# Performance work log

Hardware: AMD Instinct MI355X
Metric: run time of the kernel (lower is better)

Reference implementation:

```python
import jax, jax.numpy as jnp
import numpy as np

B, N, H, F_IN, F_OUT = 2048, 64, 4, 256, 256
NEG_SLOPE = 0.2


def setup_inputs() -> dict:
    key = jax.random.key(0)
    k1, k2, k3, k4 = jax.random.split(key, 4)
    return {
        "input": jax.random.normal(k1, (B, N, F_IN), dtype=jnp.float32),
        "adj": jax.random.uniform(k2, (B, N, N), dtype=jnp.float32),
        "W": jax.random.normal(k3, (F_IN, H * F_OUT), dtype=jnp.float32) * 0.05,
        "a_i": jax.random.normal(k4, (H, F_OUT), dtype=jnp.float32) * 0.05,
        "a_j": jax.random.normal(jax.random.fold_in(key, 5), (H, F_OUT), dtype=jnp.float32) * 0.05,
        "bias_param": jnp.zeros((H * F_OUT,), dtype=jnp.float32),
    }


def reference(input, adj, W, a_i, a_j, bias_param):
    # h: [B, N, H, F_OUT]
    h = (input @ W).reshape(B, N, H, F_OUT)
    # per-head attention coefficients (vectorized over heads)
    coeff_i = jnp.einsum("bnhf,hf->bnh", h, a_i)  # [B, N, H]
    coeff_j = jnp.einsum("bnhf,hf->bnh", h, a_j)  # [B, N, H]
    # e: [B, N(i), N(j), H]
    e = jax.nn.leaky_relu(coeff_i[:, :, None, :] + coeff_j[:, None, :, :],
                          negative_slope=NEG_SLOPE)
    adj4 = adj[..., None]  # [B, N, N, 1]
    # self_loop_type == 2: adj unchanged. Mask logits, softmax over j, re-mask.
    attention = jax.nn.softmax(e * adj4, axis=2) * adj4
    # dropout p = 0.0 / eval mode -> identity
    # weighted aggregate per head, then concat heads (average=False)
    out = jnp.einsum("bijh,bjhf->bihf", attention, h).reshape(B, N, H * F_OUT)
    return out + bias_param
```

## Files before the change

### kernel.cpp

```cpp
#include <hip/hip_runtime.h>

#define B_  2048
#define N_  64
#define H_  4
#define FI  256
#define FO  256
#define HF  1024

typedef _Float16 f16;
typedef _Float16 f16x8 __attribute__((ext_vector_type(8)));
typedef _Float16 f16x4 __attribute__((ext_vector_type(4)));
typedef float f32x4 __attribute__((ext_vector_type(4)));

#define MFMA16(a,b,c) __builtin_amdgcn_mfma_f32_16x16x32_f16(a, b, c, 0, 0, 0)

__global__ __launch_bounds__(256) void prep_w_kernel(const float* __restrict__ W,
                                                     f16* __restrict__ wfrag) {
    int tid  = blockIdx.x * 256 + threadIdx.x;
    int lane = tid & 63;
    int ctg  = (tid >> 6) & 63;
    int kt   = tid >> 12;
    int krow = kt * 32 + (lane >> 4) * 8;
    int col  = ctg * 16 + (lane & 15);
    f16x8 v;
#pragma unroll
    for (int j = 0; j < 8; ++j)
        v[j] = (f16)W[(size_t)(krow + j) * HF + col];
    *((f16x8*)wfrag + tid) = v;
}

#define SMEM_BYTES 51200
#define SADJ_OFF   32768
#define SCI_OFF    40960
#define SCJ_OFF    45056
#define SCIS_OFF   49152
#define SCJS_OFF   50176

__global__ __launch_bounds__(1024, 1) void gat_kernel(
    const float* __restrict__ input, const float* __restrict__ adj,
    const f16* __restrict__ wfrag, const float* __restrict__ a_i,
    const float* __restrict__ a_j, const float* __restrict__ bias,
    float* __restrict__ out)
{
    __shared__ unsigned char smem[SMEM_BYTES] __attribute__((aligned(16)));
    float* sCi  = (float*)(smem + SCI_OFF);
    float* sCj  = (float*)(smem + SCJ_OFF);
    float* sCiS = (float*)(smem + SCIS_OFF);
    float* sCjS = (float*)(smem + SCJS_OFF);

    const int b    = blockIdx.x;
    const int tid  = threadIdx.x;
    const int wv   = tid >> 6;
    const int w    = wv >> 2;
    const int ch2  = wv & 3;
    const int lane = tid & 63;
    const int g    = lane >> 4;
    const int c15  = lane & 15;

    {
        const float* inb = input + (size_t)b * (N_ * FI);
#pragma unroll
        for (int c = 0; c < 2; ++c) {
            int idx = tid + 1024 * c;
            int row = idx >> 5;
            int k0  = (idx & 31) << 3;
            const float4* p = (const float4*)(inb + row * FI + k0);
            float4 v0 = p[0], v1 = p[1];
            f16x8 h8;
            h8[0] = (f16)v0.x; h8[1] = (f16)v0.y; h8[2] = (f16)v0.z; h8[3] = (f16)v0.w;
            h8[4] = (f16)v1.x; h8[5] = (f16)v1.y; h8[6] = (f16)v1.z; h8[7] = (f16)v1.w;
            unsigned addr = (unsigned)(row * 512 + k0 * 2) ^ ((unsigned)(row & 7) << 4);
            *(f16x8*)(smem + addr) = h8;
        }
        if (tid < 512) {
            int i  = tid >> 3;
            int jb = tid & 7;
            const float* ap = adj + (size_t)b * (N_ * N_) + i * N_ + jb * 8;
            float4 q0 = ((const float4*)ap)[0];
            float4 q1 = ((const float4*)ap)[1];
            f16x4 lo, hi;
            lo[0] = (f16)q0.x; lo[1] = (f16)q0.y; lo[2] = (f16)q0.z; lo[3] = (f16)q0.w;
            hi[0] = (f16)q1.x; hi[1] = (f16)q1.y; hi[2] = (f16)q1.z; hi[3] = (f16)q1.w;
            unsigned k0p = (unsigned)(32 * (jb >> 2) + 16 * (jb & 1) + 4 * ((jb >> 1) & 1));
            unsigned sw  = (unsigned)(i & 7) << 4;
            *(f16x4*)(smem + SADJ_OFF + (((unsigned)(i * 128) + k0p * 2) ^ sw)) = lo;
            *(f16x4*)(smem + SADJ_OFF + (((unsigned)(i * 128) + (k0p + 8) * 2) ^ sw)) = hi;
        }
    }
    __syncthreads();

    float ciP[16], cjP[16];
#pragma unroll
    for (int q = 0; q < 16; ++q) { ciP[q] = 0.f; cjP[q] = 0.f; }
    f16x8 hB[2][4];

#pragma unroll
    for (int cc = 0; cc < 2; ++cc) {
        f32x4 acc[4][2];
#pragma unroll
        for (int rt = 0; rt < 4; ++rt)
#pragma unroll
            for (int ctl = 0; ctl < 2; ++ctl) {
                f32x4 z = {0.f, 0.f, 0.f, 0.f};
                acc[rt][ctl] = z;
            }
#pragma unroll
        for (int kt = 0; kt < 8; ++kt) {
            f16x8 aF[4];
#pragma unroll
            for (int rt = 0; rt < 4; ++rt) {
                int row = rt * 16 + c15;
                unsigned addr = ((unsigned)(row * 512 + (kt * 32 + g * 8) * 2))
                                ^ ((unsigned)(row & 7) << 4);
                aF[rt] = *(const f16x8*)(smem + addr);
            }
            f16x8 bF[2];
#pragma unroll
            for (int ctl = 0; ctl < 2; ++ctl) {
                int ctg = w * 16 + ch2 * 4 + cc * 2 + ctl;
                bF[ctl] = *((const f16x8*)wfrag + ((kt * 64 + ctg) * 64 + lane));
            }
#pragma unroll
            for (int rt = 0; rt < 4; ++rt)
#pragma unroll
                for (int ctl = 0; ctl < 2; ++ctl)
                    acc[rt][ctl] = MFMA16(aF[rt], bF[ctl], acc[rt][ctl]);
        }
#pragma unroll
        for (int ctl = 0; ctl < 2; ++ctl) {
            int ct = cc * 2 + ctl;
            int colg = w * FO + ch2 * 64 + ct * 16 + c15;
            float aIc = a_i[colg];
            float aJc = a_j[colg];
#pragma unroll
            for (int rt = 0; rt < 4; ++rt) {
#pragma unroll
                for (int r = 0; r < 4; ++r) {
                    float v = acc[rt][ctl][r];
                    ciP[rt * 4 + r] += v * aIc;
                    cjP[rt * 4 + r] += v * aJc;
                    hB[rt >> 1][ct][4 * (rt & 1) + r] = (f16)v;
                }
            }
        }
    }

#pragma unroll
    for (int s = 1; s < 16; s <<= 1) {
#pragma unroll
        for (int q = 0; q < 16; ++q) {
            ciP[q] += __shfl_xor(ciP[q], s);
            cjP[q] += __shfl_xor(cjP[q], s);
        }
    }
    if (c15 == 0) {
#pragma unroll
        for (int q = 0; q < 16; ++q) {
            int node = (q >> 2) * 16 + g * 4 + (q & 3);
            sCi[wv * 64 + node] = ciP[q];
            sCj[wv * 64 + node] = cjP[q];
        }
    }
    __syncthreads();

    if (tid < 512) {
        int wq    = tid >> 7;
        int which = (tid >> 6) & 1;
        int node  = tid & 63;
        const float* src = (which == 0 ? sCi : sCj) + (wq * 4) * 64 + node;
        float s = src[0] + src[64] + src[128] + src[192];
        (which == 0 ? sCiS : sCjS)[wq * 64 + node] = s;
    }
    __syncthreads();

#pragma unroll 1
    for (int it = 0; it < 4; ++it) {
        int i = it * 16 + c15;
        float ci = sCiS[w * 64 + i];
        unsigned sw = (unsigned)(i & 7) << 4;
        f16x8 adjv0 = *(const f16x8*)(smem + SADJ_OFF + (((unsigned)(i * 128) + (g * 8) * 2) ^ sw));
        f16x8 adjv1 = *(const f16x8*)(smem + SADJ_OFF + (((unsigned)(i * 128) + (32 + g * 8) * 2) ^ sw));
        float cj[16];
#pragma unroll
        for (int t = 0; t < 4; ++t) {
            float4 c4 = *(const float4*)(sCjS + w * 64 + t * 16 + 4 * g);
            cj[t * 4 + 0] = c4.x; cj[t * 4 + 1] = c4.y;
            cj[t * 4 + 2] = c4.z; cj[t * 4 + 3] = c4.w;
        }
        float sv[16], av[16];
#pragma unroll
        for (int q = 0; q < 16; ++q)
            av[q] = (float)(q < 8 ? adjv0[q & 7] : adjv1[q & 7]);
        float m = -1e30f;
#pragma unroll
        for (int q = 0; q < 16; ++q) {
            float e = ci + cj[q];
            e = fmaxf(e, 0.2f * e);
            float s = e * av[q];
            sv[q] = s;
            m = fmaxf(m, s);
        }
        m = fmaxf(m, __shfl_xor(m, 16));
        m = fmaxf(m, __shfl_xor(m, 32));
        float sum = 0.f;
#pragma unroll
        for (int q = 0; q < 16; ++q) { float p = __expf(sv[q] - m); sv[q] = p; sum += p; }
        sum += __shfl_xor(sum, 16);
        sum += __shfl_xor(sum, 32);
        float rs = 1.0f / sum;
        f16x8 atF[2];
#pragma unroll
        for (int jj = 0; jj < 8; ++jj) {
            atF[0][jj] = (f16)(sv[jj] * rs * av[jj]);
            atF[1][jj] = (f16)(sv[8 + jj] * rs * av[8 + jj]);
        }
        f32x4 acc2[4];
#pragma unroll
        for (int ct = 0; ct < 4; ++ct) {
            f32x4 z = {0.f, 0.f, 0.f, 0.f};
            acc2[ct] = z;
        }
#pragma unroll
        for (int kt2 = 0; kt2 < 2; ++kt2)
#pragma unroll
            for (int ct = 0; ct < 4; ++ct)
                acc2[ct] = MFMA16(atF[kt2], hB[kt2][ct], acc2[ct]);
#pragma unroll
        for (int ct = 0; ct < 4; ++ct) {
            int colg = w * FO + ch2 * 64 + ct * 16 + c15;
            float bv = bias[colg];
#pragma unroll
            for (int r = 0; r < 4; ++r) {
                int row = it * 16 + g * 4 + r;
                out[((size_t)b * N_ + row) * HF + colg] = acc2[ct][r] + bv;
            }
        }
    }
}

extern "C" void kernel_launch(void* const* d_in, const int* in_sizes, int n_in,
                              void* d_out, int out_size, void* d_ws, size_t ws_size,
                              hipStream_t stream) {
    const float* input = (const float*)d_in[0];
    const float* adj   = (const float*)d_in[1];
    const float* W     = (const float*)d_in[2];
    const float* a_i   = (const float*)d_in[3];
    const float* a_j   = (const float*)d_in[4];
    const float* bias  = (const float*)d_in[5];
    float* outp  = (float*)d_out;
    f16*   wfrag = (f16*)d_ws;

    prep_w_kernel<<<128, 256, 0, stream>>>(W, wfrag);
    gat_kernel<<<B_, 1024, 0, stream>>>(input, adj, wfrag, a_i, a_j, bias, outp);
}
```

Baseline: 262.5 us.

## Make GAT kernel persistent over 8 batches with double-buffered prefetch

Each block now processes 8 consecutive batch elements instead of one. The next batch's input and adjacency loads are issued into registers while the current batch computes, then written into an alternating shared-memory buffer. This is meant to hide global load latency and amortize block launch costs. The trade-off is shared memory nearly doubling, so fewer blocks can be resident and the grid shrinks to 256 blocks.

```diff
diff --git a/kernel.cpp b/kernel.cpp
--- a/kernel.cpp
+++ b/kernel.cpp
@@ -6,6 +6,8 @@
 #define FI  256
 #define FO  256
 #define HF  1024
+#define NB  8
+#define GRID (B_ / NB)
 
 typedef _Float16 f16;
 typedef _Float16 f16x8 __attribute__((ext_vector_type(8)));
@@ -29,12 +31,12 @@
     *((f16x8*)wfrag + tid) = v;
 }
 
-#define SMEM_BYTES 51200
-#define SADJ_OFF   32768
-#define SCI_OFF    40960
-#define SCJ_OFF    45056
-#define SCIS_OFF   49152
-#define SCJS_OFF   50176
+#define SMEM_BYTES 92160
+#define SADJ_OFF   65536
+#define SCI_OFF    81920
+#define SCJ_OFF    86016
+#define SCIS_OFF   90112
+#define SCJS_OFF   91136
 
 __global__ __launch_bounds__(1024, 1) void gat_kernel(
     const float* __restrict__ input, const float* __restrict__ adj,
@@ -48,7 +50,6 @@
     float* sCiS = (float*)(smem + SCIS_OFF);
     float* sCjS = (float*)(smem + SCJS_OFF);
 
-    const int b    = blockIdx.x;
     const int tid  = threadIdx.x;
     const int wv   = tid >> 6;
     const int w    = wv >> 2;
@@ -57,182 +58,218 @@
     const int g    = lane >> 4;
     const int c15  = lane & 15;
 
-    {
-        const float* inb = input + (size_t)b * (N_ * FI);
-#pragma unroll
-        for (int c = 0; c < 2; ++c) {
-            int idx = tid + 1024 * c;
-            int row = idx >> 5;
-            int k0  = (idx & 31) << 3;
-            const float4* p = (const float4*)(inb + row * FI + k0);
-            float4 v0 = p[0], v1 = p[1];
-            f16x8 h8;
-            h8[0] = (f16)v0.x; h8[1] = (f16)v0.y; h8[2] = (f16)v0.z; h8[3] = (f16)v0.w;
-            h8[4] = (f16)v1.x; h8[5] = (f16)v1.y; h8[6] = (f16)v1.z; h8[7] = (f16)v1.w;
-            unsigned addr = (unsigned)(row * 512 + k0 * 2) ^ ((unsigned)(row & 7) << 4);
-            *(f16x8*)(smem + addr) = h8;
-        }
-        if (tid < 512) {
-            int i  = tid >> 3;
-            int jb = tid & 7;
-            const float* ap = adj + (size_t)b * (N_ * N_) + i * N_ + jb * 8;
-            float4 q0 = ((const float4*)ap)[0];
-            float4 q1 = ((const float4*)ap)[1];
-            f16x4 lo, hi;
-            lo[0] = (f16)q0.x; lo[1] = (f16)q0.y; lo[2] = (f16)q0.z; lo[3] = (f16)q0.w;
-            hi[0] = (f16)q1.x; hi[1] = (f16)q1.y; hi[2] = (f16)q1.z; hi[3] = (f16)q1.w;
-            unsigned k0p = (unsigned)(32 * (jb >> 2) + 16 * (jb & 1) + 4 * ((jb >> 1) & 1));
-            unsigned sw  = (unsigned)(i & 7) << 4;
-            *(f16x4*)(smem + SADJ_OFF + (((unsigned)(i * 128) + k0p * 2) ^ sw)) = lo;
-            *(f16x4*)(smem + SADJ_OFF + (((unsigned)(i * 128) + (k0p + 8) * 2) ^ sw)) = hi;
-        }
-    }
-    __syncthreads();
-
-    float ciP[16], cjP[16];
-#pragma unroll
-    for (int q = 0; q < 16; ++q) { ciP[q] = 0.f; cjP[q] = 0.f; }
-    f16x8 hB[2][4];
-
-#pragma unroll
-    for (int cc = 0; cc < 2; ++cc) {
-        f32x4 acc[4][2];
-#pragma unroll
-        for (int rt = 0; rt < 4; ++rt)
+    const int srow = tid >> 5;
+    const int sk0  = (tid & 31) << 3;
+    const int ai   = tid >> 3;
+    const int ajb  = tid & 7;
+
+    const int b0 = blockIdx.x * NB;
+
+    float4 fA0, fA1, fA2, fA3;
+    float4 fJ0, fJ1;
+    f16x8 pA0, pA1;
+    f16x4 pJlo, pJhi;
+
+    auto issue_loads = [&](int bb) {
+        const float* p0 = input + (size_t)bb * (N_ * FI) + srow * FI + sk0;
+        const float* p1 = p0 + 32 * FI;
+        fA0 = ((const float4*)p0)[0];
+        fA1 = ((const float4*)p0)[1];
+        fA2 = ((const float4*)p1)[0];
+        fA3 = ((const float4*)p1)[1];
+        if (tid < 512) {
+            const float* ap = adj + (size_t)bb * (N_ * N_) + ai * N_ + ajb * 8;
+            fJ0 = ((const float4*)ap)[0];
+            fJ1 = ((const float4*)ap)[1];
+        }
+    };
+    auto convert_prefetch = [&]() {
+        pA0[0] = (f16)fA0.x; pA0[1] = (f16)fA0.y; pA0[2] = (f16)fA0.z; pA0[3] = (f16)fA0.w;
+        pA0[4] = (f16)fA1.x; pA0[5] = (f16)fA1.y; pA0[6] = (f16)fA1.z; pA0[7] = (f16)fA1.w;
+        pA1[0] = (f16)fA2.x; pA1[1] = (f16)fA2.y; pA1[2] = (f16)fA2.z; pA1[3] = (f16)fA2.w;
+        pA1[4] = (f16)fA3.x; pA1[5] = (f16)fA3.y; pA1[6] = (f16)fA3.z; pA1[7] = (f16)fA3.w;
+        if (tid < 512) {
+            pJlo[0] = (f16)fJ0.x; pJlo[1] = (f16)fJ0.y; pJlo[2] = (f16)fJ0.z; pJlo[3] = (f16)fJ0.w;
+            pJhi[0] = (f16)fJ1.x; pJhi[1] = (f16)fJ1.y; pJhi[2] = (f16)fJ1.z; pJhi[3] = (f16)fJ1.w;
+        }
+    };
+    auto write_batch = [&](int buf) {
+        unsigned bufA = (unsigned)buf * 32768u;
+        unsigned a0 = bufA + ((unsigned)(srow * 512 + sk0 * 2) ^ ((unsigned)(srow & 7) << 4));
+        *(f16x8*)(smem + a0) = pA0;
+        int srow1 = srow + 32;
+        unsigned a1 = bufA + ((unsigned)(srow1 * 512 + sk0 * 2) ^ ((unsigned)(srow1 & 7) << 4));
+        *(f16x8*)(smem + a1) = pA1;
+        if (tid < 512) {
+            unsigned bufJ = SADJ_OFF + (unsigned)buf * 8192u;
+            unsigned k0p = (unsigned)(32 * (ajb >> 2) + 16 * (ajb & 1) + 4 * ((ajb >> 1) & 1));
+            unsigned sw  = (unsigned)(ai & 7) << 4;
+            *(f16x4*)(smem + bufJ + (((unsigned)(ai * 128) + k0p * 2) ^ sw)) = pJlo;
+            *(f16x4*)(smem + bufJ + (((unsigned)(ai * 128) + (k0p + 8) * 2) ^ sw)) = pJhi;
+        }
+    };
+
+    issue_loads(b0);
+    convert_prefetch();
+
+#pragma unroll 1
+    for (int ib = 0; ib < NB; ++ib) {
+        const int b   = b0 + ib;
+        const int buf = ib & 1;
+        const unsigned bufA = (unsigned)buf * 32768u;
+        const unsigned bufJ = SADJ_OFF + (unsigned)buf * 8192u;
+
+        write_batch(buf);
+        __syncthreads();
+
+        if (ib + 1 < NB) issue_loads(b0 + ib + 1);
+
+        float ciP[16], cjP[16];
+#pragma unroll
+        for (int q = 0; q < 16; ++q) { ciP[q] = 0.f; cjP[q] = 0.f; }
+        f16x8 hB[2][4];
+
+#pragma unroll
+        for (int cc = 0; cc < 2; ++cc) {
+            f32x4 acc[4][2];
+#pragma unroll
+            for (int rt = 0; rt < 4; ++rt)
+#pragma unroll
+                for (int ctl = 0; ctl < 2; ++ctl) {
+                    f32x4 z = {0.f, 0.f, 0.f, 0.f};
+                    acc[rt][ctl] = z;
+                }
+#pragma unroll
+            for (int kt = 0; kt < 8; ++kt) {
+                f16x8 aF[4];
+#pragma unroll
+                for (int rt = 0; rt < 4; ++rt) {
+                    int row = rt * 16 + c15;
+                    unsigned addr = bufA + (((unsigned)(row * 512 + (kt * 32 + g * 8) * 2))
+                                            ^ ((unsigned)(row & 7) << 4));
+                    aF[rt] = *(const f16x8*)(smem + addr);
+                }
+                f16x8 bF[2];
+#pragma unroll
+                for (int ctl = 0; ctl < 2; ++ctl) {
+                    int ctg = w * 16 + ch2 * 4 + cc * 2 + ctl;
+                    bF[ctl] = *((const f16x8*)wfrag + ((kt * 64 + ctg) * 64 + lane));
+                }
+#pragma unroll
+                for (int rt = 0; rt < 4; ++rt)
+#pragma unroll
+                    for (int ctl = 0; ctl < 2; ++ctl)
+                        acc[rt][ctl] = MFMA16(aF[rt], bF[ctl], acc[rt][ctl]);
+            }
 #pragma unroll
             for (int ctl = 0; ctl < 2; ++ctl) {
+                int ct = cc * 2 + ctl;
+                int colg = w * FO + ch2 * 64 + ct * 16 + c15;
+                float aIc = a_i[colg];
+                float aJc = a_j[colg];
+#pragma unroll
+                for (int rt = 0; rt < 4; ++rt) {
+#pragma unroll
+                    for (int r = 0; r < 4; ++r) {
+                        float v = acc[rt][ctl][r];
+                        ciP[rt * 4 + r] += v * aIc;
+                        cjP[rt * 4 + r] += v * aJc;
+                        hB[rt >> 1][ct][4 * (rt & 1) + r] = (f16)v;
+                    }
+                }
+            }
+            if (cc == 0 && ib + 1 < NB) convert_prefetch();
+        }
+
+#pragma unroll
+        for (int s = 1; s < 16; s <<= 1) {
+#pragma unroll
+            for (int q = 0; q < 16; ++q) {
+                ciP[q] += __shfl_xor(ciP[q], s);
+                cjP[q] += __shfl_xor(cjP[q], s);
+            }
+        }
+        if (c15 == 0) {
+#pragma unroll
+            for (int q = 0; q < 16; ++q) {
+                int node = (q >> 2) * 16 + g * 4 + (q & 3);
+                sCi[wv * 64 + node] = ciP[q];
+                sCj[wv * 64 + node] = cjP[q];
+            }
+        }
+        __syncthreads();
+
+        if (tid < 512) {
+            int wq    = tid >> 7;
+            int which = (tid >> 6) & 1;
+            int node  = tid & 63;
+            const float* src = (which == 0 ? sCi : sCj) + (wq * 4) * 64 + node;
+            float s = src[0] + src[64] + src[128] + src[192];
+            (which == 0 ? sCiS : sCjS)[wq * 64 + node] = s;
+        }
+        __syncthreads();
+
+#pragma unroll 1
+        for (int it = 0; it < 4; ++it) {
+            int i = it * 16 + c15;
+            float ci = sCiS[w * 64 + i];
+            unsigned sw = (unsigned)(i & 7) << 4;
+            f16x8 adjv0 = *(const f16x8*)(smem + bufJ + (((unsigned)(i * 128) + (g * 8) * 2) ^ sw));
+            f16x8 adjv1 = *(const f16x8*)(smem + bufJ + (((unsigned)(i * 128) + (32 + g * 8) * 2) ^ sw));
+            float cj[16];
+#pragma unroll
+            for (int t = 0; t < 4; ++t) {
+                float4 c4 = *(const float4*)(sCjS + w * 64 + t * 16 + 4 * g);
+                cj[t * 4 + 0] = c4.x; cj[t * 4 + 1] = c4.y;
+                cj[t * 4 + 2] = c4.z; cj[t * 4 + 3] = c4.w;
+            }
+            float sv[16], av[16];
+#pragma unroll
+            for (int q = 0; q < 16; ++q)
+                av[q] = (float)(q < 8 ? adjv0[q & 7] : adjv1[q & 7]);
+            float m = -1e30f;
+#pragma unroll
+            for (int q = 0; q < 16; ++q) {
+                float e = ci + cj[q];
+                e = fmaxf(e, 0.2f * e);
+                float s = e * av[q];
+                sv[q] = s;
+                m = fmaxf(m, s);
+            }
+            m = fmaxf(m, __shfl_xor(m, 16));
+            m = fmaxf(m, __shfl_xor(m, 32));
+            float sum = 0.f;
+#pragma unroll
+            for (int q = 0; q < 16; ++q) { float p = __expf(sv[q] - m); sv[q] = p; sum += p; }
+            sum += __shfl_xor(sum, 16);
+            sum += __shfl_xor(sum, 32);
+            float rs = 1.0f / sum;
+            f16x8 atF[2];
+#pragma unroll
+            for (int jj = 0; jj < 8; ++jj) {
+                atF[0][jj] = (f16)(sv[jj] * rs * av[jj]);
+                atF[1][jj] = (f16)(sv[8 + jj] * rs * av[8 + jj]);
+            }
+            f32x4 acc2[4];
+#pragma unroll
+            for (int ct = 0; ct < 4; ++ct) {
                 f32x4 z = {0.f, 0.f, 0.f, 0.f};
-                acc[rt][ctl] = z;
-            }
-#pragma unroll
-        for (int kt = 0; kt < 8; ++kt) {
-            f16x8 aF[4];
-#pragma unroll
-            for (int rt = 0; rt < 4; ++rt) {
-                int row = rt * 16 + c15;
-                unsigned addr = ((unsigned)(row * 512 + (kt * 32 + g * 8) * 2))
-                                ^ ((unsigned)(row & 7) << 4);
-                aF[rt] = *(const f16x8*)(smem + addr);
-            }
-            f16x8 bF[2];
-#pragma unroll
-            for (int ctl = 0; ctl < 2; ++ctl) {
-                int ctg = w * 16 + ch2 * 4 + cc * 2 + ctl;
-                bF[ctl] = *((const f16x8*)wfrag + ((kt * 64 + ctg) * 64 + lane));
-            }
-#pragma unroll
-            for (int rt = 0; rt < 4; ++rt)
-#pragma unroll
-                for (int ctl = 0; ctl < 2; ++ctl)
-                    acc[rt][ctl] = MFMA16(aF[rt], bF[ctl], acc[rt][ctl]);
-        }
-#pragma unroll
-        for (int ctl = 0; ctl < 2; ++ctl) {
-            int ct = cc * 2 + ctl;
-            int colg = w * FO + ch2 * 64 + ct * 16 + c15;
-            float aIc = a_i[colg];
-            float aJc = a_j[colg];
-#pragma unroll
-            for (int rt = 0; rt < 4; ++rt) {
+                acc2[ct] = z;
+            }
+#pragma unroll
+            for (int kt2 = 0; kt2 < 2; ++kt2)
+#pragma unroll
+                for (int ct = 0; ct < 4; ++ct)
+                    acc2[ct] = MFMA16(atF[kt2], hB[kt2][ct], acc2[ct]);
+#pragma unroll
+            for (int ct = 0; ct < 4; ++ct) {
+                int colg = w * FO + ch2 * 64 + ct * 16 + c15;
+                float bv = bias[colg];
 #pragma unroll
                 for (int r = 0; r < 4; ++r) {
-                    float v = acc[rt][ctl][r];
-                    ciP[rt * 4 + r] += v * aIc;
-                    cjP[rt * 4 + r] += v * aJc;
-                    hB[rt >> 1][ct][4 * (rt & 1) + r] = (f16)v;
-                }
-            }
-        }
-    }
-
-#pragma unroll
-    for (int s = 1; s < 16; s <<= 1) {
-#pragma unroll
-        for (int q = 0; q < 16; ++q) {
-            ciP[q] += __shfl_xor(ciP[q], s);
-            cjP[q] += __shfl_xor(cjP[q], s);
-        }
-    }
-    if (c15 == 0) {
-#pragma unroll
-        for (int q = 0; q < 16; ++q) {
-            int node = (q >> 2) * 16 + g * 4 + (q & 3);
-            sCi[wv * 64 + node] = ciP[q];
-            sCj[wv * 64 + node] = cjP[q];
-        }
-    }
-    __syncthreads();
-
-    if (tid < 512) {
-        int wq    = tid >> 7;
-        int which = (tid >> 6) & 1;
-        int node  = tid & 63;
-        const float* src = (which == 0 ? sCi : sCj) + (wq * 4) * 64 + node;
-        float s = src[0] + src[64] + src[128] + src[192];
-        (which == 0 ? sCiS : sCjS)[wq * 64 + node] = s;
-    }
-    __syncthreads();
-
-#pragma unroll 1
-    for (int it = 0; it < 4; ++it) {
-        int i = it * 16 + c15;
-        float ci = sCiS[w * 64 + i];
-        unsigned sw = (unsigned)(i & 7) << 4;
-        f16x8 adjv0 = *(const f16x8*)(smem + SADJ_OFF + (((unsigned)(i * 128) + (g * 8) * 2) ^ sw));
-        f16x8 adjv1 = *(const f16x8*)(smem + SADJ_OFF + (((unsigned)(i * 128) + (32 + g * 8) * 2) ^ sw));
-        float cj[16];
-#pragma unroll
-        for (int t = 0; t < 4; ++t) {
-            float4 c4 = *(const float4*)(sCjS + w * 64 + t * 16 + 4 * g);
-            cj[t * 4 + 0] = c4.x; cj[t * 4 + 1] = c4.y;
-            cj[t * 4 + 2] = c4.z; cj[t * 4 + 3] = c4.w;
-        }
-        float sv[16], av[16];
-#pragma unroll
-        for (int q = 0; q < 16; ++q)
-            av[q] = (float)(q < 8 ? adjv0[q & 7] : adjv1[q & 7]);
-        float m = -1e30f;
-#pragma unroll
-        for (int q = 0; q < 16; ++q) {
-            float e = ci + cj[q];
-            e = fmaxf(e, 0.2f * e);
-            float s = e * av[q];
-            sv[q] = s;
-            m = fmaxf(m, s);
-        }
-        m = fmaxf(m, __shfl_xor(m, 16));
-        m = fmaxf(m, __shfl_xor(m, 32));
-        float sum = 0.f;
-#pragma unroll
-        for (int q = 0; q < 16; ++q) { float p = __expf(sv[q] - m); sv[q] = p; sum += p; }
-        sum += __shfl_xor(sum, 16);
-        sum += __shfl_xor(sum, 32);
-        float rs = 1.0f / sum;
-        f16x8 atF[2];
-#pragma unroll
-        for (int jj = 0; jj < 8; ++jj) {
-            atF[0][jj] = (f16)(sv[jj] * rs * av[jj]);
-            atF[1][jj] = (f16)(sv[8 + jj] * rs * av[8 + jj]);
-        }
-        f32x4 acc2[4];
-#pragma unroll
-        for (int ct = 0; ct < 4; ++ct) {
-            f32x4 z = {0.f, 0.f, 0.f, 0.f};
-            acc2[ct] = z;
-        }
-#pragma unroll
-        for (int kt2 = 0; kt2 < 2; ++kt2)
-#pragma unroll
-            for (int ct = 0; ct < 4; ++ct)
-                acc2[ct] = MFMA16(atF[kt2], hB[kt2][ct], acc2[ct]);
-#pragma unroll
-        for (int ct = 0; ct < 4; ++ct) {
-            int colg = w * FO + ch2 * 64 + ct * 16 + c15;
-            float bv = bias[colg];
-#pragma unroll
-            for (int r = 0; r < 4; ++r) {
-                int row = it * 16 + g * 4 + r;
-                out[((size_t)b * N_ + row) * HF + colg] = acc2[ct][r] + bv;
+                    int row = it * 16 + g * 4 + r;
+                    out[((size_t)b * N_ + row) * HF + colg] = acc2[ct][r] + bv;
+                }
             }
         }
     }
@@ -251,5 +288,5 @@
     f16*   wfrag = (f16*)d_ws;
 
     prep_w_kernel<<<128, 256, 0, stream>>>(W, wfrag);
-    gat_kernel<<<B_, 1024, 0, stream>>>(input, adj, wfrag, a_i, a_j, bias, outp);
+    gat_kernel<<<GRID, 1024, 0, stream>>>(input, adj, wfrag, a_i, a_j, bias, outp);
 }
```

After: 726.4 us. 177% more time.
